# Optimization experiments

Hardware: AMD Instinct MI355X
Metric: run time of the kernel (lower is better)

## Reference

```python
import jax, jax.numpy as jnp
import numpy as np

K = 5  # unfold kernel size
PAD = 2  # unfold padding (zeros)
PENALTY = 1.5


def setup_inputs() -> dict:
    key = jax.random.key(0)
    k1, k2 = jax.random.split(key)
    x = jax.random.normal(k1, (8, 21, 512, 512), dtype=jnp.float32)
    y = jax.random.randint(k2, (8, 512, 512), 0, 21, dtype=jnp.int32)
    return {"x": x, "y": y}


def reference(x, y):
    # x: [B, C, W, H] logits; y: [B, W, H] integer labels
    xm = jnp.argmax(x, axis=1)  # [B, W, H] predicted class per pixel
    B, W, H = xm.shape
    xm = xm.astype(y.dtype)
    # nn.Unfold(kernel_size=5, padding=2) zero-pads y, then compares each of the
    # 25 shifted neighbor maps against argmax. Instead of materializing the
    y_pad = jnp.pad(y, ((0, 0), (PAD, PAD), (PAD, PAD)))  # zero padding like Unfold
    count = jnp.zeros((B, W, H), dtype=jnp.float32)
    for di in range(K):
        for dj in range(K):
            count = count + (y_pad[:, di:di + W, dj:dj + H] != xm).astype(jnp.float32)
    weight = 1.0 + PENALTY * count  # ones_like(y) with += 1.5 per mismatching neighbor
    return weight[:, None, :, :]  # [B, 1, W, H]
```

## Files before the change

### kernel.cpp

```cpp
#include <hip/hip_runtime.h>


typedef float f32x4 __attribute__((ext_vector_type(4)));
typedef int   i32x4 __attribute__((ext_vector_type(4)));

constexpr int B = 8;
constexpr int C = 21;
constexpr int W = 512;
constexpr int H = 512;
constexpr int PIX = W * H;

__global__ __launch_bounds__(256, 4) void getweight_kernel(
    const float* __restrict__ x, const int* __restrict__ y,
    float* __restrict__ out)
{
    const int tid = blockIdx.x * blockDim.x + threadIdx.x;
    const int gpr = H / 4;
    const int gpi = W * gpr;
    const int b   = tid / gpi;
    const int rem = tid - b * gpi;
    const int w   = rem / gpr;
    const int h   = (rem - w * gpr) << 2;

    const float* xp = x + (size_t)b * C * PIX + (size_t)w * H + h;
    f32x4 best = __builtin_nontemporal_load((const f32x4*)xp);
    int am0 = 0, am1 = 0, am2 = 0, am3 = 0;

#define ARGMAX_STEP(v, c)                                      \
    do {                                                       \
        if ((v)[0] > best[0]) { best[0] = (v)[0]; am0 = (c); } \
        if ((v)[1] > best[1]) { best[1] = (v)[1]; am1 = (c); } \
        if ((v)[2] > best[2]) { best[2] = (v)[2]; am2 = (c); } \
        if ((v)[3] > best[3]) { best[3] = (v)[3]; am3 = (c); } \
    } while (0)

#pragma unroll
    for (int g = 0; g < 5; ++g) {
        const int c0 = 4 * g + 1;
        f32x4 v0 = __builtin_nontemporal_load((const f32x4*)(xp + (size_t)(c0 + 0) * PIX));
        f32x4 v1 = __builtin_nontemporal_load((const f32x4*)(xp + (size_t)(c0 + 1) * PIX));
        f32x4 v2 = __builtin_nontemporal_load((const f32x4*)(xp + (size_t)(c0 + 2) * PIX));
        f32x4 v3 = __builtin_nontemporal_load((const f32x4*)(xp + (size_t)(c0 + 3) * PIX));
        ARGMAX_STEP(v0, c0 + 0);
        ARGMAX_STEP(v1, c0 + 1);
        ARGMAX_STEP(v2, c0 + 2);
        ARGMAX_STEP(v3, c0 + 3);
    }
#undef ARGMAX_STEP

    const int* yb = y + b * PIX;
    const i32x4 zero4 = {0, 0, 0, 0};
    int cnt0 = 0, cnt1 = 0, cnt2 = 0, cnt3 = 0;
#pragma unroll
    for (int di = 0; di < 5; ++di) {
        const int ww = w + di - 2;
        const bool wok = (unsigned)ww < (unsigned)W;
        const int* yrow = yb + ww * H;
        i32x4 ca = (wok && h >= 4)       ? *(const i32x4*)(yrow + h - 4) : zero4;
        i32x4 cb = wok                   ? *(const i32x4*)(yrow + h)     : zero4;
        i32x4 cc = (wok && h <= H - 8)   ? *(const i32x4*)(yrow + h + 4) : zero4;
        const int yr[12] = {ca[0], ca[1], ca[2], ca[3],
                            cb[0], cb[1], cb[2], cb[3],
                            cc[0], cc[1], cc[2], cc[3]};
#pragma unroll
        for (int dj = 0; dj < 5; ++dj) {
            cnt0 += (yr[2 + 0 + dj] != am0) ? 1 : 0;
            cnt1 += (yr[2 + 1 + dj] != am1) ? 1 : 0;
            cnt2 += (yr[2 + 2 + dj] != am2) ? 1 : 0;
            cnt3 += (yr[2 + 3 + dj] != am3) ? 1 : 0;
        }
    }

    f32x4 res;
    res[0] = 1.0f + 1.5f * (float)cnt0;
    res[1] = 1.0f + 1.5f * (float)cnt1;
    res[2] = 1.0f + 1.5f * (float)cnt2;
    res[3] = 1.0f + 1.5f * (float)cnt3;
    __builtin_nontemporal_store(res, (f32x4*)(out + (size_t)b * PIX + (size_t)w * H + h));
}

extern "C" void kernel_launch(void* const* d_in, const int* in_sizes, int n_in,
                              void* d_out, int out_size, void* d_ws, size_t ws_size,
                              hipStream_t stream) {
    const float* x = (const float*)d_in[0];
    const int*   y = (const int*)d_in[1];
    float* out = (float*)d_out;

    const int total_threads = B * PIX / 4;
    const int block = 256;
    const int grid = total_threads / block;
    getweight_kernel<<<grid, block, 0, stream>>>(x, y, out);
}
```

Baseline: 249.0 us.

## Split fused argmax+neighbor-count kernel into two kernels via packed workspace map

Separates the channel argmax into its own kernel that writes a byte-packed argmax map to workspace, followed by a second kernel that reads the map and computes the 5x5 neighbor mismatch weights. The argmax kernel uses higher occupancy launch bounds to better stream the large logits tensor. This adds a second launch and an extra round trip of the packed map through memory, and falls back to the fused kernel when no workspace is provided.

```diff
diff --git a/kernel.cpp b/kernel.cpp
--- a/kernel.cpp
+++ b/kernel.cpp
@@ -9,8 +9,96 @@
 constexpr int W = 512;
 constexpr int H = 512;
 constexpr int PIX = W * H;
+constexpr int NGROUP = B * PIX / 4;
 
-__global__ __launch_bounds__(256, 4) void getweight_kernel(
+__global__ __launch_bounds__(256, 8) void argmax_kernel(
+    const float* __restrict__ x, unsigned int* __restrict__ amap)
+{
+    const int tid = blockIdx.x * blockDim.x + threadIdx.x;
+    const int gpi = PIX / 4;
+    const int b   = tid / gpi;
+    const int g   = tid - b * gpi;
+
+    const float* xp = x + (size_t)b * C * PIX + (size_t)g * 4;
+    f32x4 best = __builtin_nontemporal_load((const f32x4*)xp);
+    int am0 = 0, am1 = 0, am2 = 0, am3 = 0;
+
+#define ARGMAX_STEP(v, c)                                      \
+    do {                                                       \
+        if ((v)[0] > best[0]) { best[0] = (v)[0]; am0 = (c); } \
+        if ((v)[1] > best[1]) { best[1] = (v)[1]; am1 = (c); } \
+        if ((v)[2] > best[2]) { best[2] = (v)[2]; am2 = (c); } \
+        if ((v)[3] > best[3]) { best[3] = (v)[3]; am3 = (c); } \
+    } while (0)
+
+#pragma unroll
+    for (int grp = 0; grp < 5; ++grp) {
+        const int c0 = 4 * grp + 1;
+        f32x4 v0 = __builtin_nontemporal_load((const f32x4*)(xp + (size_t)(c0 + 0) * PIX));
+        f32x4 v1 = __builtin_nontemporal_load((const f32x4*)(xp + (size_t)(c0 + 1) * PIX));
+        f32x4 v2 = __builtin_nontemporal_load((const f32x4*)(xp + (size_t)(c0 + 2) * PIX));
+        f32x4 v3 = __builtin_nontemporal_load((const f32x4*)(xp + (size_t)(c0 + 3) * PIX));
+        ARGMAX_STEP(v0, c0 + 0);
+        ARGMAX_STEP(v1, c0 + 1);
+        ARGMAX_STEP(v2, c0 + 2);
+        ARGMAX_STEP(v3, c0 + 3);
+    }
+#undef ARGMAX_STEP
+
+    amap[tid] = (unsigned int)am0 | ((unsigned int)am1 << 8) |
+                ((unsigned int)am2 << 16) | ((unsigned int)am3 << 24);
+}
+
+__global__ __launch_bounds__(256, 4) void weight_kernel(
+    const unsigned int* __restrict__ amap, const int* __restrict__ y,
+    float* __restrict__ out)
+{
+    const int tid = blockIdx.x * blockDim.x + threadIdx.x;
+    const int gpr = H / 4;
+    const int gpi = W * gpr;
+    const int b   = tid / gpi;
+    const int rem = tid - b * gpi;
+    const int w   = rem / gpr;
+    const int h   = (rem - w * gpr) << 2;
+
+    const unsigned int packed = amap[tid];
+    const int am0 = (int)(packed & 0xFFu);
+    const int am1 = (int)((packed >> 8) & 0xFFu);
+    const int am2 = (int)((packed >> 16) & 0xFFu);
+    const int am3 = (int)((packed >> 24) & 0xFFu);
+
+    const int* yb = y + b * PIX;
+    const i32x4 zero4 = {0, 0, 0, 0};
+    int cnt0 = 0, cnt1 = 0, cnt2 = 0, cnt3 = 0;
+#pragma unroll
+    for (int di = 0; di < 5; ++di) {
+        const int ww = w + di - 2;
+        const bool wok = (unsigned)ww < (unsigned)W;
+        const int* yrow = yb + ww * H;
+        i32x4 ca = (wok && h >= 4)     ? *(const i32x4*)(yrow + h - 4) : zero4;
+        i32x4 cb = wok                 ? *(const i32x4*)(yrow + h)     : zero4;
+        i32x4 cc = (wok && h <= H - 8) ? *(const i32x4*)(yrow + h + 4) : zero4;
+        const int yr[12] = {ca[0], ca[1], ca[2], ca[3],
+                            cb[0], cb[1], cb[2], cb[3],
+                            cc[0], cc[1], cc[2], cc[3]};
+#pragma unroll
+        for (int dj = 0; dj < 5; ++dj) {
+            cnt0 += (yr[2 + 0 + dj] != am0) ? 1 : 0;
+            cnt1 += (yr[2 + 1 + dj] != am1) ? 1 : 0;
+            cnt2 += (yr[2 + 2 + dj] != am2) ? 1 : 0;
+            cnt3 += (yr[2 + 3 + dj] != am3) ? 1 : 0;
+        }
+    }
+
+    f32x4 res;
+    res[0] = 1.0f + 1.5f * (float)cnt0;
+    res[1] = 1.0f + 1.5f * (float)cnt1;
+    res[2] = 1.0f + 1.5f * (float)cnt2;
+    res[3] = 1.0f + 1.5f * (float)cnt3;
+    __builtin_nontemporal_store(res, (f32x4*)(out + (size_t)b * PIX + (size_t)w * H + h));
+}
+
+__global__ __launch_bounds__(256, 4) void getweight_fused(
     const float* __restrict__ x, const int* __restrict__ y,
     float* __restrict__ out)
 {
@@ -25,7 +113,6 @@
     const float* xp = x + (size_t)b * C * PIX + (size_t)w * H + h;
     f32x4 best = __builtin_nontemporal_load((const f32x4*)xp);
     int am0 = 0, am1 = 0, am2 = 0, am3 = 0;
-
 #define ARGMAX_STEP(v, c)                                      \
     do {                                                       \
         if ((v)[0] > best[0]) { best[0] = (v)[0]; am0 = (c); } \
@@ -33,7 +120,6 @@
         if ((v)[2] > best[2]) { best[2] = (v)[2]; am2 = (c); } \
         if ((v)[3] > best[3]) { best[3] = (v)[3]; am3 = (c); } \
     } while (0)
-
 #pragma unroll
     for (int g = 0; g < 5; ++g) {
         const int c0 = 4 * g + 1;
@@ -56,9 +142,9 @@
         const int ww = w + di - 2;
         const bool wok = (unsigned)ww < (unsigned)W;
         const int* yrow = yb + ww * H;
-        i32x4 ca = (wok && h >= 4)       ? *(const i32x4*)(yrow + h - 4) : zero4;
-        i32x4 cb = wok                   ? *(const i32x4*)(yrow + h)     : zero4;
-        i32x4 cc = (wok && h <= H - 8)   ? *(const i32x4*)(yrow + h + 4) : zero4;
+        i32x4 ca = (wok && h >= 4)     ? *(const i32x4*)(yrow + h - 4) : zero4;
+        i32x4 cb = wok                 ? *(const i32x4*)(yrow + h)     : zero4;
+        i32x4 cc = (wok && h <= H - 8) ? *(const i32x4*)(yrow + h + 4) : zero4;
         const int yr[12] = {ca[0], ca[1], ca[2], ca[3],
                             cb[0], cb[1], cb[2], cb[3],
                             cc[0], cc[1], cc[2], cc[3]};
@@ -86,8 +172,14 @@
     const int*   y = (const int*)d_in[1];
     float* out = (float*)d_out;
 
-    const int total_threads = B * PIX / 4;
     const int block = 256;
-    const int grid = total_threads / block;
-    getweight_kernel<<<grid, block, 0, stream>>>(x, y, out);
+    const int grid = NGROUP / block;
+
+    if (d_ws != nullptr && ws_size >= (size_t)NGROUP * sizeof(unsigned int)) {
+        unsigned int* amap = (unsigned int*)d_ws;
+        argmax_kernel<<<grid, block, 0, stream>>>(x, amap);
+        weight_kernel<<<grid, block, 0, stream>>>(amap, y, out);
+    } else {
+        getweight_fused<<<grid, block, 0, stream>>>(x, y, out);
+    }
 }
```

New measurement: 238.6 us. -4.2%, faster.
